# Performance work log

Measured on AMD Instinct MI355X. Metric: run time of the kernel, lower is better.

## Reference

```python
import jax, jax.numpy as jnp
import numpy as np

B, T, H, L2 = 131072, 4, 8, 5  # T=4 forced by conv1 in_channels=4; L2 = layers 1..5 of the 6-layer lstm1


def _lstm_dir(xs, w_ih, w_hh, b, h0, c0):
    # xs: [T, B, Din] -> hs: [T, B, H]; PyTorch gate order i, f, g, o
    def step(carry, xt):
        h, c = carry
        g = xt @ w_ih.T + h @ w_hh.T + b
        i, f, gg, o = jnp.split(g, 4, axis=-1)
        c = jax.nn.sigmoid(f) * c + jax.nn.sigmoid(i) * jnp.tanh(gg)
        h = jax.nn.sigmoid(o) * jnp.tanh(c)
        return (h, c), h
    _, hs = jax.lax.scan(step, (h0, c0), xs)
    return hs


def _bilstm(xs, wi_f, wh_f, b_f, wi_b, wh_b, b_b, h0f, c0f, h0b, c0b):
    hf = _lstm_dir(xs, wi_f, wh_f, b_f, h0f, c0f)
    hb = _lstm_dir(xs[::-1], wi_b, wh_b, b_b, h0b, c0b)[::-1]
    return jnp.concatenate([hf, hb], axis=-1)  # [T, B, 2H]


def _conv1d(x, w, b):
    # x: [B, C, L], w: [O, I, K] (torch Conv1d layout)
    y = jax.lax.conv_general_dilated(x, w, (1,), [(0, 0)], dimension_numbers=('NCH', 'OIH', 'NCH'))
    return y + b[None, :, None]


def _deconv1d(x, w, b):
    # torch ConvTranspose1d weight [I, O, K]; stride 1, pad 0 == full conv with flipped kernel
    k = w.shape[-1]
    wk = jnp.flip(jnp.swapaxes(w, 0, 1), -1)  # [O, I, K]
    y = jax.lax.conv_general_dilated(x, wk, (1,), [(k - 1, k - 1)], dimension_numbers=('NCH', 'OIH', 'NCH'))
    return y + b[None, :, None]


def setup_inputs():
    key = jax.random.key(0)
    ks = iter(jax.random.split(key, 32))
    rn = lambda shape, s=0.2: jax.random.normal(next(ks), shape, jnp.float32) * s
    return {
        'x': rn((B, T, 2), 1.0),
        'h0': rn((12, B, H), 1.0),
        'c0': rn((12, B, H), 1.0),
        'w_ih0': rn((2, 4 * H, 2)),
        'w_hh0': rn((2, 4 * H, H)),
        'b_ih0': rn((2, 4 * H)),
        'b_hh0': rn((2, 4 * H)),
        'w_ih': rn((L2, 2, 4 * H, 2 * H)),
        'w_hh': rn((L2, 2, 4 * H, H)),
        'b_ih': rn((L2, 2, 4 * H)),
        'b_hh': rn((L2, 2, 4 * H)),
        'conv1_w': rn((8, 4, 2)), 'conv1_b': rn((8,)),
        'conv2_w': rn((16, 8, 2)), 'conv2_b': rn((16,)),
        'deconv1_w': rn((16, 8, 2)), 'deconv1_b': rn((8,)),
        'deconv2_w': rn((8, 4, 2)), 'deconv2_b': rn((4,)),
        'fc1_w': rn((8, 16)), 'fc1_b': rn((8,)),
        'fc2_w': rn((4, 8)), 'fc2_b': rn((4,)),
    }


def reference(x, h0, c0, w_ih0, w_hh0, b_ih0, b_hh0, w_ih, w_hh, b_ih, b_hh,
              conv1_w, conv1_b, conv2_w, conv2_b, deconv1_w, deconv1_b,
              deconv2_w, deconv2_b, fc1_w, fc1_b, fc2_w, fc2_b):
    xs = jnp.swapaxes(x, 0, 1)  # [T, B, 2]
    y = _bilstm(xs, w_ih0[0], w_hh0[0], b_ih0[0] + b_hh0[0],
                w_ih0[1], w_hh0[1], b_ih0[1] + b_hh0[1],
                h0[0], c0[0], h0[1], c0[1])
    for l in range(L2):  # fixed, small layer count (eval mode: inter-layer dropout off)
        i = 2 * (l + 1)
        y = _bilstm(y, w_ih[l, 0], w_hh[l, 0], b_ih[l, 0] + b_hh[l, 0],
                    w_ih[l, 1], w_hh[l, 1], b_ih[l, 1] + b_hh[l, 1],
                    h0[i], c0[i], h0[i + 1], c0[i + 1])
    y = jax.nn.sigmoid(jnp.swapaxes(y, 0, 1))  # [B, 4, 16]; dim 1 acts as conv channels
    y = _conv1d(y, conv1_w, conv1_b)           # [B, 8, 15]
    y = _conv1d(y, conv2_w, conv2_b)           # [B, 16, 14]
    y = _deconv1d(y, deconv1_w, deconv1_b)     # [B, 8, 15]
    y = _deconv1d(y, deconv2_w, deconv2_b)     # [B, 4, 16]
    y = y @ fc1_w.T + fc1_b                    # [B, 4, 8]
    y = y @ fc2_w.T + fc2_b                    # [B, 4, 4]
    return jnp.tanh(y)
```

## Files before the change

### kernel.cpp

```cpp
#include <hip/hip_runtime.h>
#include <hip/hip_bf16.h>


using f32x2 = __attribute__((ext_vector_type(2))) float;
using f32x4 = __attribute__((ext_vector_type(4))) float;

#define OFF_WIH0 0
#define OFF_WHH0 128
#define OFF_B0   640
#define OFF_WIH  704
#define OFF_WHH  5824
#define OFF_B    8384
#define OFF_M    9024
#define OFF_MB   10048

__device__ __forceinline__ float rcpf_(float x) {
#if __has_builtin(__builtin_amdgcn_rcpf)
    return __builtin_amdgcn_rcpf(x);
#else
    return 1.0f / x;
#endif
}
__device__ __forceinline__ float exp2f_(float x) {
#if __has_builtin(__builtin_amdgcn_exp2f)
    return __builtin_amdgcn_exp2f(x);
#else
    return exp2f(x);
#endif
}
__device__ __forceinline__ float sigm(float x) {
    return rcpf_(1.0f + exp2f_(-1.44269504f * x));
}
__device__ __forceinline__ float tanhx(float x) {
    return fmaf(2.0f, rcpf_(1.0f + exp2f_(-2.88539008f * x)), -1.0f);
}

__global__ __launch_bounds__(256) void prep_all(
    const float* __restrict__ wih0, const float* __restrict__ whh0,
    const float* __restrict__ bih0, const float* __restrict__ bhh0,
    const float* __restrict__ wih,  const float* __restrict__ whh,
    const float* __restrict__ bih,  const float* __restrict__ bhh,
    const float* __restrict__ c1w, const float* __restrict__ c1b,
    const float* __restrict__ c2w, const float* __restrict__ c2b,
    const float* __restrict__ d1w, const float* __restrict__ d1b,
    const float* __restrict__ d2w, const float* __restrict__ d2b,
    const float* __restrict__ f1w, const float* __restrict__ f1b,
    const float* __restrict__ f2w, const float* __restrict__ f2b,
    float* __restrict__ W)
{
    __shared__ float A[13][232];
    __shared__ float Bf[13][232];
    const int tid = threadIdx.x;

    if (blockIdx.x < 36) {
        int t = blockIdx.x * 256 + tid;
        const int n = 36 * 256;
        for (int i = t; i < 128; i += n)  W[OFF_WIH0 + i] = wih0[i];
        for (int i = t; i < 512; i += n)  W[OFF_WHH0 + i] = whh0[i];
        for (int i = t; i < 64; i += n)   W[OFF_B0 + i] = bih0[i] + bhh0[i];
        for (int i = t; i < 5120; i += n) W[OFF_WIH + i] = wih[i];
        for (int i = t; i < 2560; i += n) W[OFF_WHH + i] = whh[i];
        for (int i = t; i < 640; i += n)  W[OFF_B + i] = bih[i] + bhh[i];
        return;
    }
    const int base = (blockIdx.x - 36) * 13;

    for (int idx = tid; idx < 13 * 64; idx += 256) {
        int cl = idx / 64, r = idx % 64;
        A[cl][r] = (base + cl == r) ? 1.0f : 0.0f;
    }
    __syncthreads();
    for (int idx = tid; idx < 13 * 120; idx += 256) {
        int cl = idx / 120, rr = idx % 120; int o = rr / 15, l = rr % 15;
        float acc = (base + cl == 64) ? c1b[o] : 0.0f;
        for (int i = 0; i < 4; i++)
            for (int kk = 0; kk < 2; kk++)
                acc += c1w[(o * 4 + i) * 2 + kk] * A[cl][i * 16 + l + kk];
        Bf[cl][rr] = acc;
    }
    __syncthreads();
    for (int idx = tid; idx < 13 * 224; idx += 256) {
        int cl = idx / 224, rr = idx % 224; int o = rr / 14, l = rr % 14;
        float acc = (base + cl == 64) ? c2b[o] : 0.0f;
        for (int i = 0; i < 8; i++)
            for (int kk = 0; kk < 2; kk++)
                acc += c2w[(o * 8 + i) * 2 + kk] * Bf[cl][i * 15 + l + kk];
        A[cl][rr] = acc;
    }
    __syncthreads();
    for (int idx = tid; idx < 13 * 120; idx += 256) {
        int cl = idx / 120, rr = idx % 120; int o = rr / 15, l = rr % 15;
        float acc = (base + cl == 64) ? d1b[o] : 0.0f;
        for (int i = 0; i < 16; i++)
            for (int kk = 0; kk < 2; kk++) {
                int ls = l - kk;
                if (ls >= 0 && ls < 14)
                    acc += d1w[(i * 8 + o) * 2 + kk] * A[cl][i * 14 + ls];
            }
        Bf[cl][rr] = acc;
    }
    __syncthreads();
    for (int idx = tid; idx < 13 * 64; idx += 256) {
        int cl = idx / 64, rr = idx % 64; int o = rr / 16, l = rr % 16;
        float acc = (base + cl == 64) ? d2b[o] : 0.0f;
        for (int i = 0; i < 8; i++)
            for (int kk = 0; kk < 2; kk++) {
                int ls = l - kk;
                if (ls >= 0 && ls < 15)
                    acc += d2w[(i * 4 + o) * 2 + kk] * Bf[cl][i * 15 + ls];
            }
        A[cl][rr] = acc;
    }
    __syncthreads();
    for (int idx = tid; idx < 13 * 32; idx += 256) {
        int cl = idx / 32, rr = idx % 32; int ch = rr / 8, jj = rr % 8;
        float acc = (base + cl == 64) ? f1b[jj] : 0.0f;
        for (int l = 0; l < 16; l++)
            acc += f1w[jj * 16 + l] * A[cl][ch * 16 + l];
        Bf[cl][rr] = acc;
    }
    __syncthreads();
    for (int idx = tid; idx < 13 * 16; idx += 256) {
        int cl = idx / 16, rr = idx % 16; int ch = rr / 4, m = rr % 4;
        int col = base + cl;
        if (col > 64) continue;
        float acc = (col == 64) ? f2b[m] : 0.0f;
        for (int j = 0; j < 8; j++)
            acc += f2w[m * 8 + j] * Bf[cl][ch * 8 + j];
        if (col < 64) W[OFF_M + rr * 64 + col] = acc;
        else          W[OFF_MB + rr] = acc;
    }
}

template<bool FWD>
__device__ __forceinline__ void layer16(
    const float* __restrict__ Wi, const float* __restrict__ Wh,
    const float* __restrict__ Bs,
    const float* __restrict__ h0s, const float* __restrict__ c0s,
    int elem0, int u, int bbase,
    float* const (&lin)[4], float* const (&lout)[4], bool last)
{
    f32x4 wiv[4][4];
    f32x4 whv[4][2];
    f32x4 bsv;
#pragma unroll
    for (int g = 0; g < 4; g++) {
        const int r = u + 8 * g;
        const f32x4* wr = reinterpret_cast<const f32x4*>(Wi + r * 16);
        wiv[g][0] = wr[0]; wiv[g][1] = wr[1]; wiv[g][2] = wr[2]; wiv[g][3] = wr[3];
        const f32x4* ur = reinterpret_cast<const f32x4*>(Wh + r * 8);
        whv[g][0] = ur[0]; whv[g][1] = ur[1];
        bsv[g] = Bs[r];
    }

    float hin[4][8];
    float cc[4];
#pragma unroll
    for (int e = 0; e < 4; e++) {
        const f32x4* hp = reinterpret_cast<const f32x4*>(h0s + (size_t)(elem0 + e) * 8);
        f32x4 a = hp[0], b = hp[1];
        hin[e][0] = a.x; hin[e][1] = a.y; hin[e][2] = a.z; hin[e][3] = a.w;
        hin[e][4] = b.x; hin[e][5] = b.y; hin[e][6] = b.z; hin[e][7] = b.w;
        cc[e] = c0s[(size_t)(elem0 + e) * 8 + u];
    }

#pragma unroll
    for (int s = 0; s < 4; s++) {
        const int t = FWD ? s : 3 - s;
        f32x2 acc[4][4];
#pragma unroll
        for (int e = 0; e < 4; e++) {
            const f32x4* ip = reinterpret_cast<const f32x4*>(lin[e] + 16 * t);
            f32x4 i0 = ip[0], i1 = ip[1], i2 = ip[2], i3 = ip[3];
            f32x2 xin[8];
            xin[0] = f32x2{i0.x, i0.y}; xin[1] = f32x2{i0.z, i0.w};
            xin[2] = f32x2{i1.x, i1.y}; xin[3] = f32x2{i1.z, i1.w};
            xin[4] = f32x2{i2.x, i2.y}; xin[5] = f32x2{i2.z, i2.w};
            xin[6] = f32x2{i3.x, i3.y}; xin[7] = f32x2{i3.z, i3.w};
#pragma unroll
            for (int g = 0; g < 4; g++) {
                f32x2 a = f32x2{bsv[g], 0.0f};
#pragma unroll
                for (int j = 0; j < 4; j++) {
                    f32x2 wlo = f32x2{wiv[g][j].x, wiv[g][j].y};
                    f32x2 whi = f32x2{wiv[g][j].z, wiv[g][j].w};
                    a = __builtin_elementwise_fma(xin[2 * j], wlo, a);
                    a = __builtin_elementwise_fma(xin[2 * j + 1], whi, a);
                }
                acc[e][g] = a;
            }
        }
#pragma unroll
        for (int g = 0; g < 4; g++) {
#pragma unroll
            for (int j = 0; j < 2; j++) {
                f32x2 wlo = f32x2{whv[g][j].x, whv[g][j].y};
                f32x2 whi = f32x2{whv[g][j].z, whv[g][j].w};
#pragma unroll
                for (int e = 0; e < 4; e++) {
                    f32x2 h0p = f32x2{hin[e][4 * j], hin[e][4 * j + 1]};
                    f32x2 h1p = f32x2{hin[e][4 * j + 2], hin[e][4 * j + 3]};
                    acc[e][g] = __builtin_elementwise_fma(h0p, wlo, acc[e][g]);
                    acc[e][g] = __builtin_elementwise_fma(h1p, whi, acc[e][g]);
                }
            }
        }
        float hn[4];
#pragma unroll
        for (int e = 0; e < 4; e++) {
            float si = sigm(acc[e][0].x + acc[e][0].y);
            float sf = sigm(acc[e][1].x + acc[e][1].y);
            float tg = tanhx(acc[e][2].x + acc[e][2].y);
            float so = sigm(acc[e][3].x + acc[e][3].y);
            cc[e] = fmaf(sf, cc[e], si * tg);
            hn[e] = so * tanhx(cc[e]);
        }
#pragma unroll
        for (int e = 0; e < 4; e++)
#pragma unroll
            for (int k = 0; k < 8; k++)
                hin[e][k] = __int_as_float(
                    __builtin_amdgcn_ds_bpermute(bbase + 4 * k, __float_as_int(hn[e])));
#pragma unroll
        for (int e = 0; e < 4; e++)
            lout[e][16 * t + (FWD ? 0 : 8) + u] = last ? sigm(hn[e]) : hn[e];
    }
}

template<bool FWD>
__device__ __forceinline__ void layer2(
    const float* __restrict__ Wi, const float* __restrict__ Wh,
    const float* __restrict__ Bs,
    const float* __restrict__ h0s, const float* __restrict__ c0s,
    int elem0, int u, int bbase,
    const f32x2 (&xin2)[4][4], float* const (&lout)[4])
{
    f32x2 wiv[4];
    f32x4 whv[4][2];
    f32x4 bsv;
#pragma unroll
    for (int g = 0; g < 4; g++) {
        const int r = u + 8 * g;
        wiv[g] = *reinterpret_cast<const f32x2*>(Wi + r * 2);
        const f32x4* ur = reinterpret_cast<const f32x4*>(Wh + r * 8);
        whv[g][0] = ur[0]; whv[g][1] = ur[1];
        bsv[g] = Bs[r];
    }
    float hin[4][8];
    float cc[4];
#pragma unroll
    for (int e = 0; e < 4; e++) {
        const f32x4* hp = reinterpret_cast<const f32x4*>(h0s + (size_t)(elem0 + e) * 8);
        f32x4 a = hp[0], b = hp[1];
        hin[e][0] = a.x; hin[e][1] = a.y; hin[e][2] = a.z; hin[e][3] = a.w;
        hin[e][4] = b.x; hin[e][5] = b.y; hin[e][6] = b.z; hin[e][7] = b.w;
        cc[e] = c0s[(size_t)(elem0 + e) * 8 + u];
    }

#pragma unroll
    for (int s = 0; s < 4; s++) {
        const int t = FWD ? s : 3 - s;
        f32x2 acc[4][4];
#pragma unroll
        for (int e = 0; e < 4; e++)
#pragma unroll
            for (int g = 0; g < 4; g++)
                acc[e][g] = __builtin_elementwise_fma(xin2[e][t], wiv[g], f32x2{bsv[g], 0.0f});
#pragma unroll
        for (int g = 0; g < 4; g++)
#pragma unroll
            for (int j = 0; j < 2; j++) {
                f32x2 wlo = f32x2{whv[g][j].x, whv[g][j].y};
                f32x2 whi = f32x2{whv[g][j].z, whv[g][j].w};
#pragma unroll
                for (int e = 0; e < 4; e++) {
                    f32x2 h0p = f32x2{hin[e][4 * j], hin[e][4 * j + 1]};
                    f32x2 h1p = f32x2{hin[e][4 * j + 2], hin[e][4 * j + 3]};
                    acc[e][g] = __builtin_elementwise_fma(h0p, wlo, acc[e][g]);
                    acc[e][g] = __builtin_elementwise_fma(h1p, whi, acc[e][g]);
                }
            }
        float hn[4];
#pragma unroll
        for (int e = 0; e < 4; e++) {
            float si = sigm(acc[e][0].x + acc[e][0].y);
            float sf = sigm(acc[e][1].x + acc[e][1].y);
            float tg = tanhx(acc[e][2].x + acc[e][2].y);
            float so = sigm(acc[e][3].x + acc[e][3].y);
            cc[e] = fmaf(sf, cc[e], si * tg);
            hn[e] = so * tanhx(cc[e]);
        }
#pragma unroll
        for (int e = 0; e < 4; e++)
#pragma unroll
            for (int k = 0; k < 8; k++)
                hin[e][k] = __int_as_float(
                    __builtin_amdgcn_ds_bpermute(bbase + 4 * k, __float_as_int(hn[e])));
#pragma unroll
        for (int e = 0; e < 4; e++)
            lout[e][16 * t + (FWD ? 0 : 8) + u] = hn[e];
    }
}

__global__ __launch_bounds__(128, 2) void lstm_main(
    const float* __restrict__ x, const float* __restrict__ h0,
    const float* __restrict__ c0, const float* __restrict__ W,
    float* __restrict__ out, int B)
{
    __shared__ float yb[2][64 * 68];
    const int tid = threadIdx.x;
    const int lane = tid & 63;
    const int u = lane & 7;
    const int slot = tid >> 3;
    const int elem0 = blockIdx.x * 64 + slot * 4;
    const int bbase = (lane & 56) << 2;

    float* y0[4]; float* y1[4];
#pragma unroll
    for (int e = 0; e < 4; e++) {
        y0[e] = &yb[0][(slot * 4 + e) * 68];
        y1[e] = &yb[1][(slot * 4 + e) * 68];
    }

    f32x2 xin2[4][4];
#pragma unroll
    for (int e = 0; e < 4; e++) {
        const f32x4* xp = reinterpret_cast<const f32x4*>(x + (size_t)(elem0 + e) * 8);
        f32x4 a = xp[0], b = xp[1];
        xin2[e][0] = f32x2{a.x, a.y}; xin2[e][1] = f32x2{a.z, a.w};
        xin2[e][2] = f32x2{b.x, b.y}; xin2[e][3] = f32x2{b.z, b.w};
    }

    layer2<true>(W + OFF_WIH0, W + OFF_WHH0, W + OFF_B0,
                 h0 + (size_t)0 * B * 8, c0 + (size_t)0 * B * 8,
                 elem0, u, bbase, xin2, y0);
    layer2<false>(W + OFF_WIH0 + 64, W + OFF_WHH0 + 256, W + OFF_B0 + 32,
                  h0 + (size_t)1 * B * 8, c0 + (size_t)1 * B * 8,
                  elem0, u, bbase, xin2, y0);

#pragma unroll
    for (int l = 1; l <= 5; l++) {
        float* const (&lin)[4] = (l & 1) ? y0 : y1;
        float* const (&lout)[4] = (l & 1) ? y1 : y0;
        const float* wi = W + OFF_WIH + (size_t)(l - 1) * 1024;
        const float* wh = W + OFF_WHH + (size_t)(l - 1) * 512;
        const float* bb = W + OFF_B + (size_t)(l - 1) * 64;
        const int slotIdx = 2 * l;
        const bool last = (l == 5);
        layer16<true>(wi, wh, bb,
                      h0 + (size_t)slotIdx * B * 8, c0 + (size_t)slotIdx * B * 8,
                      elem0, u, bbase, lin, lout, last);
        layer16<false>(wi + 512, wh + 256, bb + 32,
                       h0 + (size_t)(slotIdx + 1) * B * 8, c0 + (size_t)(slotIdx + 1) * B * 8,
                       elem0, u, bbase, lin, lout, last);
    }

    {
        const int o0 = 2 * u, o1 = 2 * u + 1;
        const f32x4* M0 = reinterpret_cast<const f32x4*>(W + OFF_M + o0 * 64);
        const f32x4* M1 = reinterpret_cast<const f32x4*>(W + OFF_M + o1 * 64);
        const float b0 = W[OFF_MB + o0];
        const float b1 = W[OFF_MB + o1];
#pragma unroll
        for (int e = 0; e < 4; e++) {
            float a0 = b0, a1 = b1;
#pragma unroll
            for (int q = 0; q < 16; q++) {
                f32x4 sv = *reinterpret_cast<const f32x4*>(y1[e] + 4 * q);
                f32x4 m0 = M0[q], m1 = M1[q];
                a0 = fmaf(sv.x, m0.x, a0); a0 = fmaf(sv.y, m0.y, a0);
                a0 = fmaf(sv.z, m0.z, a0); a0 = fmaf(sv.w, m0.w, a0);
                a1 = fmaf(sv.x, m1.x, a1); a1 = fmaf(sv.y, m1.y, a1);
                a1 = fmaf(sv.z, m1.z, a1); a1 = fmaf(sv.w, m1.w, a1);
            }
            f32x2 res;
            res.x = tanhx(a0);
            res.y = tanhx(a1);
            *reinterpret_cast<f32x2*>(out + (size_t)(elem0 + e) * 16 + 2 * u) = res;
        }
    }
}

extern "C" void kernel_launch(void* const* d_in, const int* in_sizes, int n_in,
                              void* d_out, int out_size, void* d_ws, size_t ws_size,
                              hipStream_t stream)
{
    const float* x    = (const float*)d_in[0];
    const float* h0   = (const float*)d_in[1];
    const float* c0   = (const float*)d_in[2];
    const float* wih0 = (const float*)d_in[3];
    const float* whh0 = (const float*)d_in[4];
    const float* bih0 = (const float*)d_in[5];
    const float* bhh0 = (const float*)d_in[6];
    const float* wih  = (const float*)d_in[7];
    const float* whh  = (const float*)d_in[8];
    const float* bih  = (const float*)d_in[9];
    const float* bhh  = (const float*)d_in[10];
    const float* c1w  = (const float*)d_in[11];
    const float* c1b  = (const float*)d_in[12];
    const float* c2w  = (const float*)d_in[13];
    const float* c2b  = (const float*)d_in[14];
    const float* d1w  = (const float*)d_in[15];
    const float* d1b  = (const float*)d_in[16];
    const float* d2w  = (const float*)d_in[17];
    const float* d2b  = (const float*)d_in[18];
    const float* f1w  = (const float*)d_in[19];
    const float* f1b  = (const float*)d_in[20];
    const float* f2w  = (const float*)d_in[21];
    const float* f2b  = (const float*)d_in[22];

    float* W = (float*)d_ws;
    const int B = in_sizes[0] / 8;

    prep_all<<<41, 256, 0, stream>>>(wih0, whh0, bih0, bhh0, wih, whh, bih, bhh,
                                     c1w, c1b, c2w, c2b, d1w, d1b, d2w, d2b,
                                     f1w, f1b, f2w, f2b, W);
    lstm_main<<<B / 64, 128, 0, stream>>>(x, h0, c0, W, (float*)d_out, B);
}
```

Baseline: 380.1 us.

## Halve per-thread batch work and exchange LSTM hidden state through LDS

Each block now runs 256 threads that handle 2 batch elements each instead of 128 threads handling 4. Launch bounds move to 256 threads with 3 blocks per CU, aiming at more resident waves and lower register pressure. The 8-lane hidden-state broadcast via ds_bpermute is replaced by reading the previous step's h back from the shared layer-output buffer, relying on in-wave ordering of LDS accesses. The h-projection is fused into the same gate accumulation loop, and the last layer writes raw h and applies the sigmoid in a final pass.

```diff
diff --git a/kernel.cpp b/kernel.cpp
--- a/kernel.cpp
+++ b/kernel.cpp
@@ -132,13 +132,13 @@
     }
 }
 
-template<bool FWD>
+template<bool FWD, bool LAST>
 __device__ __forceinline__ void layer16(
     const float* __restrict__ Wi, const float* __restrict__ Wh,
     const float* __restrict__ Bs,
     const float* __restrict__ h0s, const float* __restrict__ c0s,
-    int elem0, int u, int bbase,
-    float* const (&lin)[4], float* const (&lout)[4], bool last)
+    int gelem0, int u,
+    float* const (&lin)[2], float* const (&lout)[2])
 {
     f32x4 wiv[4][4];
     f32x4 whv[4][2];
@@ -152,31 +152,40 @@
         whv[g][0] = ur[0]; whv[g][1] = ur[1];
         bsv[g] = Bs[r];
     }
-
-    float hin[4][8];
-    float cc[4];
-#pragma unroll
-    for (int e = 0; e < 4; e++) {
-        const f32x4* hp = reinterpret_cast<const f32x4*>(h0s + (size_t)(elem0 + e) * 8);
-        f32x4 a = hp[0], b = hp[1];
-        hin[e][0] = a.x; hin[e][1] = a.y; hin[e][2] = a.z; hin[e][3] = a.w;
-        hin[e][4] = b.x; hin[e][5] = b.y; hin[e][6] = b.z; hin[e][7] = b.w;
-        cc[e] = c0s[(size_t)(elem0 + e) * 8 + u];
-    }
+    f32x4 hg[2][2];
+    float cc[2];
+#pragma unroll
+    for (int e = 0; e < 2; e++) {
+        const f32x4* hp = reinterpret_cast<const f32x4*>(h0s + (size_t)(gelem0 + e) * 8);
+        hg[e][0] = hp[0]; hg[e][1] = hp[1];
+        cc[e] = c0s[(size_t)(gelem0 + e) * 8 + u];
+    }
+    float hreg[2][4];
+    const int off = FWD ? 0 : 8;
 
 #pragma unroll
     for (int s = 0; s < 4; s++) {
         const int t = FWD ? s : 3 - s;
-        f32x2 acc[4][4];
-#pragma unroll
-        for (int e = 0; e < 4; e++) {
+        const int tprev = FWD ? t - 1 : t + 1;
+        f32x2 acc[2][4];
+#pragma unroll
+        for (int e = 0; e < 2; e++) {
             const f32x4* ip = reinterpret_cast<const f32x4*>(lin[e] + 16 * t);
             f32x4 i0 = ip[0], i1 = ip[1], i2 = ip[2], i3 = ip[3];
+            f32x4 ha, hb;
+            if (s == 0) { ha = hg[e][0]; hb = hg[e][1]; }
+            else {
+                const f32x4* hp = reinterpret_cast<const f32x4*>(lout[e] + 16 * tprev + off);
+                ha = hp[0]; hb = hp[1];
+            }
             f32x2 xin[8];
             xin[0] = f32x2{i0.x, i0.y}; xin[1] = f32x2{i0.z, i0.w};
             xin[2] = f32x2{i1.x, i1.y}; xin[3] = f32x2{i1.z, i1.w};
             xin[4] = f32x2{i2.x, i2.y}; xin[5] = f32x2{i2.z, i2.w};
             xin[6] = f32x2{i3.x, i3.y}; xin[7] = f32x2{i3.z, i3.w};
+            f32x2 hx[4];
+            hx[0] = f32x2{ha.x, ha.y}; hx[1] = f32x2{ha.z, ha.w};
+            hx[2] = f32x2{hb.x, hb.y}; hx[3] = f32x2{hb.z, hb.w};
 #pragma unroll
             for (int g = 0; g < 4; g++) {
                 f32x2 a = f32x2{bsv[g], 0.0f};
@@ -187,43 +196,36 @@
                     a = __builtin_elementwise_fma(xin[2 * j], wlo, a);
                     a = __builtin_elementwise_fma(xin[2 * j + 1], whi, a);
                 }
+#pragma unroll
+                for (int j = 0; j < 2; j++) {
+                    f32x2 wlo = f32x2{whv[g][j].x, whv[g][j].y};
+                    f32x2 whi = f32x2{whv[g][j].z, whv[g][j].w};
+                    a = __builtin_elementwise_fma(hx[2 * j], wlo, a);
+                    a = __builtin_elementwise_fma(hx[2 * j + 1], whi, a);
+                }
                 acc[e][g] = a;
             }
         }
 #pragma unroll
-        for (int g = 0; g < 4; g++) {
-#pragma unroll
-            for (int j = 0; j < 2; j++) {
-                f32x2 wlo = f32x2{whv[g][j].x, whv[g][j].y};
-                f32x2 whi = f32x2{whv[g][j].z, whv[g][j].w};
-#pragma unroll
-                for (int e = 0; e < 4; e++) {
-                    f32x2 h0p = f32x2{hin[e][4 * j], hin[e][4 * j + 1]};
-                    f32x2 h1p = f32x2{hin[e][4 * j + 2], hin[e][4 * j + 3]};
-                    acc[e][g] = __builtin_elementwise_fma(h0p, wlo, acc[e][g]);
-                    acc[e][g] = __builtin_elementwise_fma(h1p, whi, acc[e][g]);
-                }
-            }
-        }
-        float hn[4];
-#pragma unroll
-        for (int e = 0; e < 4; e++) {
+        for (int e = 0; e < 2; e++) {
             float si = sigm(acc[e][0].x + acc[e][0].y);
             float sf = sigm(acc[e][1].x + acc[e][1].y);
             float tg = tanhx(acc[e][2].x + acc[e][2].y);
             float so = sigm(acc[e][3].x + acc[e][3].y);
             cc[e] = fmaf(sf, cc[e], si * tg);
-            hn[e] = so * tanhx(cc[e]);
+            float hn = so * tanhx(cc[e]);
+            lout[e][16 * t + off + u] = hn;
+            if (LAST) hreg[e][s] = hn;
         }
-#pragma unroll
-        for (int e = 0; e < 4; e++)
-#pragma unroll
-            for (int k = 0; k < 8; k++)
-                hin[e][k] = __int_as_float(
-                    __builtin_amdgcn_ds_bpermute(bbase + 4 * k, __float_as_int(hn[e])));
-#pragma unroll
-        for (int e = 0; e < 4; e++)
-            lout[e][16 * t + (FWD ? 0 : 8) + u] = last ? sigm(hn[e]) : hn[e];
+    }
+    if (LAST) {
+#pragma unroll
+        for (int e = 0; e < 2; e++)
+#pragma unroll
+            for (int s = 0; s < 4; s++) {
+                const int t = FWD ? s : 3 - s;
+                lout[e][16 * t + off + u] = sigm(hreg[e][s]);
+            }
     }
 }
 
@@ -232,8 +234,8 @@
     const float* __restrict__ Wi, const float* __restrict__ Wh,
     const float* __restrict__ Bs,
     const float* __restrict__ h0s, const float* __restrict__ c0s,
-    int elem0, int u, int bbase,
-    const f32x2 (&xin2)[4][4], float* const (&lout)[4])
+    int gelem0, int u,
+    const f32x2 (&xin2)[2][4], float* const (&lout)[2])
 {
     f32x2 wiv[4];
     f32x4 whv[4][2];
@@ -246,86 +248,80 @@
         whv[g][0] = ur[0]; whv[g][1] = ur[1];
         bsv[g] = Bs[r];
     }
-    float hin[4][8];
-    float cc[4];
-#pragma unroll
-    for (int e = 0; e < 4; e++) {
-        const f32x4* hp = reinterpret_cast<const f32x4*>(h0s + (size_t)(elem0 + e) * 8);
-        f32x4 a = hp[0], b = hp[1];
-        hin[e][0] = a.x; hin[e][1] = a.y; hin[e][2] = a.z; hin[e][3] = a.w;
-        hin[e][4] = b.x; hin[e][5] = b.y; hin[e][6] = b.z; hin[e][7] = b.w;
-        cc[e] = c0s[(size_t)(elem0 + e) * 8 + u];
-    }
+    f32x4 hg[2][2];
+    float cc[2];
+#pragma unroll
+    for (int e = 0; e < 2; e++) {
+        const f32x4* hp = reinterpret_cast<const f32x4*>(h0s + (size_t)(gelem0 + e) * 8);
+        hg[e][0] = hp[0]; hg[e][1] = hp[1];
+        cc[e] = c0s[(size_t)(gelem0 + e) * 8 + u];
+    }
+    const int off = FWD ? 0 : 8;
 
 #pragma unroll
     for (int s = 0; s < 4; s++) {
         const int t = FWD ? s : 3 - s;
-        f32x2 acc[4][4];
-#pragma unroll
-        for (int e = 0; e < 4; e++)
-#pragma unroll
-            for (int g = 0; g < 4; g++)
-                acc[e][g] = __builtin_elementwise_fma(xin2[e][t], wiv[g], f32x2{bsv[g], 0.0f});
-#pragma unroll
-        for (int g = 0; g < 4; g++)
-#pragma unroll
-            for (int j = 0; j < 2; j++) {
-                f32x2 wlo = f32x2{whv[g][j].x, whv[g][j].y};
-                f32x2 whi = f32x2{whv[g][j].z, whv[g][j].w};
-#pragma unroll
-                for (int e = 0; e < 4; e++) {
-                    f32x2 h0p = f32x2{hin[e][4 * j], hin[e][4 * j + 1]};
-                    f32x2 h1p = f32x2{hin[e][4 * j + 2], hin[e][4 * j + 3]};
-                    acc[e][g] = __builtin_elementwise_fma(h0p, wlo, acc[e][g]);
-                    acc[e][g] = __builtin_elementwise_fma(h1p, whi, acc[e][g]);
+        const int tprev = FWD ? t - 1 : t + 1;
+        f32x2 acc[2][4];
+#pragma unroll
+        for (int e = 0; e < 2; e++) {
+            f32x4 ha, hb;
+            if (s == 0) { ha = hg[e][0]; hb = hg[e][1]; }
+            else {
+                const f32x4* hp = reinterpret_cast<const f32x4*>(lout[e] + 16 * tprev + off);
+                ha = hp[0]; hb = hp[1];
+            }
+            f32x2 hx[4];
+            hx[0] = f32x2{ha.x, ha.y}; hx[1] = f32x2{ha.z, ha.w};
+            hx[2] = f32x2{hb.x, hb.y}; hx[3] = f32x2{hb.z, hb.w};
+#pragma unroll
+            for (int g = 0; g < 4; g++) {
+                f32x2 a = __builtin_elementwise_fma(xin2[e][t], wiv[g], f32x2{bsv[g], 0.0f});
+#pragma unroll
+                for (int j = 0; j < 2; j++) {
+                    f32x2 wlo = f32x2{whv[g][j].x, whv[g][j].y};
+                    f32x2 whi = f32x2{whv[g][j].z, whv[g][j].w};
+                    a = __builtin_elementwise_fma(hx[2 * j], wlo, a);
+                    a = __builtin_elementwise_fma(hx[2 * j + 1], whi, a);
                 }
-            }
-        float hn[4];
-#pragma unroll
-        for (int e = 0; e < 4; e++) {
+                acc[e][g] = a;
+            }
+        }
+#pragma unroll
+        for (int e = 0; e < 2; e++) {
             float si = sigm(acc[e][0].x + acc[e][0].y);
             float sf = sigm(acc[e][1].x + acc[e][1].y);
             float tg = tanhx(acc[e][2].x + acc[e][2].y);
             float so = sigm(acc[e][3].x + acc[e][3].y);
             cc[e] = fmaf(sf, cc[e], si * tg);
-            hn[e] = so * tanhx(cc[e]);
+            lout[e][16 * t + off + u] = so * tanhx(cc[e]);
         }
-#pragma unroll
-        for (int e = 0; e < 4; e++)
-#pragma unroll
-            for (int k = 0; k < 8; k++)
-                hin[e][k] = __int_as_float(
-                    __builtin_amdgcn_ds_bpermute(bbase + 4 * k, __float_as_int(hn[e])));
-#pragma unroll
-        for (int e = 0; e < 4; e++)
-            lout[e][16 * t + (FWD ? 0 : 8) + u] = hn[e];
-    }
-}
-
-__global__ __launch_bounds__(128, 2) void lstm_main(
+    }
+}
+
+__global__ __launch_bounds__(256, 3) void lstm_main(
     const float* __restrict__ x, const float* __restrict__ h0,
     const float* __restrict__ c0, const float* __restrict__ W,
     float* __restrict__ out, int B)
 {
     __shared__ float yb[2][64 * 68];
     const int tid = threadIdx.x;
-    const int lane = tid & 63;
-    const int u = lane & 7;
+    const int u = tid & 7;
     const int slot = tid >> 3;
-    const int elem0 = blockIdx.x * 64 + slot * 4;
-    const int bbase = (lane & 56) << 2;
-
-    float* y0[4]; float* y1[4];
-#pragma unroll
-    for (int e = 0; e < 4; e++) {
-        y0[e] = &yb[0][(slot * 4 + e) * 68];
-        y1[e] = &yb[1][(slot * 4 + e) * 68];
-    }
-
-    f32x2 xin2[4][4];
-#pragma unroll
-    for (int e = 0; e < 4; e++) {
-        const f32x4* xp = reinterpret_cast<const f32x4*>(x + (size_t)(elem0 + e) * 8);
+    const int row0 = slot * 2;
+    const int gelem0 = blockIdx.x * 64 + row0;
+
+    float* y0[2]; float* y1[2];
+#pragma unroll
+    for (int e = 0; e < 2; e++) {
+        y0[e] = &yb[0][(row0 + e) * 68];
+        y1[e] = &yb[1][(row0 + e) * 68];
+    }
+
+    f32x2 xin2[2][4];
+#pragma unroll
+    for (int e = 0; e < 2; e++) {
+        const f32x4* xp = reinterpret_cast<const f32x4*>(x + (size_t)(gelem0 + e) * 8);
         f32x4 a = xp[0], b = xp[1];
         xin2[e][0] = f32x2{a.x, a.y}; xin2[e][1] = f32x2{a.z, a.w};
         xin2[e][2] = f32x2{b.x, b.y}; xin2[e][3] = f32x2{b.z, b.w};
@@ -333,26 +329,36 @@
 
     layer2<true>(W + OFF_WIH0, W + OFF_WHH0, W + OFF_B0,
                  h0 + (size_t)0 * B * 8, c0 + (size_t)0 * B * 8,
-                 elem0, u, bbase, xin2, y0);
+                 gelem0, u, xin2, y0);
     layer2<false>(W + OFF_WIH0 + 64, W + OFF_WHH0 + 256, W + OFF_B0 + 32,
                   h0 + (size_t)1 * B * 8, c0 + (size_t)1 * B * 8,
-                  elem0, u, bbase, xin2, y0);
-
-#pragma unroll
-    for (int l = 1; l <= 5; l++) {
-        float* const (&lin)[4] = (l & 1) ? y0 : y1;
-        float* const (&lout)[4] = (l & 1) ? y1 : y0;
+                  gelem0, u, xin2, y0);
+
+#pragma unroll
+    for (int l = 1; l <= 4; l++) {
+        float* const (&lin)[2] = (l & 1) ? y0 : y1;
+        float* const (&lout)[2] = (l & 1) ? y1 : y0;
         const float* wi = W + OFF_WIH + (size_t)(l - 1) * 1024;
         const float* wh = W + OFF_WHH + (size_t)(l - 1) * 512;
         const float* bb = W + OFF_B + (size_t)(l - 1) * 64;
-        const int slotIdx = 2 * l;
-        const bool last = (l == 5);
-        layer16<true>(wi, wh, bb,
-                      h0 + (size_t)slotIdx * B * 8, c0 + (size_t)slotIdx * B * 8,
-                      elem0, u, bbase, lin, lout, last);
-        layer16<false>(wi + 512, wh + 256, bb + 32,
-                       h0 + (size_t)(slotIdx + 1) * B * 8, c0 + (size_t)(slotIdx + 1) * B * 8,
-                       elem0, u, bbase, lin, lout, last);
+        const int si = 2 * l;
+        layer16<true, false>(wi, wh, bb,
+                             h0 + (size_t)si * B * 8, c0 + (size_t)si * B * 8,
+                             gelem0, u, lin, lout);
+        layer16<false, false>(wi + 512, wh + 256, bb + 32,
+                              h0 + (size_t)(si + 1) * B * 8, c0 + (size_t)(si + 1) * B * 8,
+                              gelem0, u, lin, lout);
+    }
+    {
+        const float* wi = W + OFF_WIH + (size_t)4 * 1024;
+        const float* wh = W + OFF_WHH + (size_t)4 * 512;
+        const float* bb = W + OFF_B + (size_t)4 * 64;
+        layer16<true, true>(wi, wh, bb,
+                            h0 + (size_t)10 * B * 8, c0 + (size_t)10 * B * 8,
+                            gelem0, u, y0, y1);
+        layer16<false, true>(wi + 512, wh + 256, bb + 32,
+                             h0 + (size_t)11 * B * 8, c0 + (size_t)11 * B * 8,
+                             gelem0, u, y0, y1);
     }
 
     {
@@ -362,7 +368,7 @@
         const float b0 = W[OFF_MB + o0];
         const float b1 = W[OFF_MB + o1];
 #pragma unroll
-        for (int e = 0; e < 4; e++) {
+        for (int e = 0; e < 2; e++) {
             float a0 = b0, a1 = b1;
 #pragma unroll
             for (int q = 0; q < 16; q++) {
@@ -376,7 +382,7 @@
             f32x2 res;
             res.x = tanhx(a0);
             res.y = tanhx(a1);
-            *reinterpret_cast<f32x2*>(out + (size_t)(elem0 + e) * 16 + 2 * u) = res;
+            *reinterpret_cast<f32x2*>(out + (size_t)(gelem0 + e) * 16 + 2 * u) = res;
         }
     }
 }
@@ -415,5 +421,5 @@
     prep_all<<<41, 256, 0, stream>>>(wih0, whh0, bih0, bhh0, wih, whh, bih, bhh,
                                      c1w, c1b, c2w, c2b, d1w, d1b, d2w, d2b,
                                      f1w, f1b, f2w, f2b, W);
-    lstm_main<<<B / 64, 128, 0, stream>>>(x, h0, c0, W, (float*)d_out, B);
-}
+    lstm_main<<<B / 64, 256, 0, stream>>>(x, h0, c0, W, (float*)d_out, B);
+}
```

Measured after the change: 350.3 us. 1.08x faster.
